# Kernel optimization log

Measured on AMD Instinct MI355X. Metric: run time of the kernel, lower is better.

Reference implementation:

```python
import jax, jax.numpy as jnp
import numpy as np

N, CH, H, W = 2, 64, 96, 96
NH, CHUNK, RED = 4, 144, 4
CM = CH // RED  # match channels = 16
RES_SCALE = 1.0
NORM_EPS = 5e-5


def conv2d(x, w, b):
    # 3x3 'same' conv, NCHW / OIHW
    y = jax.lax.conv_general_dilated(x, w, (1, 1), 'SAME',
                                     dimension_numbers=('NCHW', 'OIHW', 'NCHW'))
    return y + b[None, :, None, None]


def setup_inputs() -> dict:
    key = jax.random.key(0)
    ks = jax.random.split(key, 8)
    L = H * W
    hb = min(L // CHUNK + (L // CHUNK) % 2, 128)  # = 64
    x = jax.random.normal(ks[0], (N, CH, H, W), jnp.float32)
    # per-round semi-orthogonal rotations: rows of (CM, hb) orthonormal
    g = jax.random.normal(ks[1], (NH, hb, CM), jnp.float32)
    q = jnp.stack([jnp.linalg.qr(g[h])[0] for h in range(NH)])  # (NH, hb, CM)
    rot = jnp.transpose(q, (2, 0, 1))  # (CM, NH, hb)
    def s(k, shape, fan):
        return jax.random.normal(k, shape, jnp.float32) / np.sqrt(fan).astype(np.float32)
    wm = s(ks[2], (CM, CH, 3, 3), CH * 9)
    wa = s(ks[3], (CH, CH, 3, 3), CH * 9)
    wf = s(ks[4], (CH, CH, 3, 3), CH * 9)
    fc1_w = s(ks[5], (CHUNK, CH), CH)
    fc2_w = s(ks[6], (CHUNK, CHUNK), CHUNK)
    return {'x': x, 'rot': rot,
            'wm': wm, 'bm': jnp.zeros((CM,), jnp.float32),
            'wa': wa, 'ba': jnp.zeros((CH,), jnp.float32),
            'wf': wf, 'bf': jnp.zeros((CH,), jnp.float32),
            'fc1_w': fc1_w, 'fc1_b': jnp.zeros((CHUNK,), jnp.float32),
            'fc2_w': fc2_w, 'fc2_b': jnp.zeros((CHUNK,), jnp.float32)}


def reference(x, rot, wm, bm, wa, ba, wf, bf, fc1_w, fc1_b, fc2_w, fc2_b):
    n, _, h, w = x.shape
    L = h * w
    hb = rot.shape[-1]
    # embeddings: (N, L, C)
    xe = jax.nn.relu(conv2d(x, wm, bm)).reshape(n, CM, L).transpose(0, 2, 1)
    ye = jax.nn.relu(conv2d(x, wa, ba)).reshape(n, CH, L).transpose(0, 2, 1)
    fe = jax.nn.relu(conv2d(x, wf, bf)).reshape(n, CH, L).transpose(0, 2, 1)
    # LSH: argmax over rotated directions, offset per round (detached in original)
    rv = jnp.einsum('ntf,fhi->nhti', xe, rot)  # (N, NH, L, hb)
    codes = jnp.argmax(rv, -1) + (jnp.arange(NH) * hb)[None, :, None]
    codes = codes.reshape(n, NH * L)
    idx = jnp.argsort(codes, axis=-1)
    undo = jnp.argsort(idx, axis=-1)
    mod = idx % L
    gather = lambda t: jnp.take_along_axis(t, mod[..., None], axis=1)
    nch = L // CHUNK  # L chosen divisible by CHUNK -> padding = 0
    xs = gather(xe).reshape(n, NH, nch, CHUNK, CM)
    ys = gather(ye).reshape(n, NH, nch, CHUNK, CH)
    fs = gather(fe).reshape(n, NH, nch, CHUNK, CH)
    nrm = jnp.linalg.norm(xs, axis=-1, keepdims=True)
    xmatch = xs / jnp.maximum(nrm, NORM_EPS)
    adj = lambda t: jnp.concatenate([t, jnp.roll(t, 1, axis=2), jnp.roll(t, -1, axis=2)], axis=3)
    xmatch = adj(xmatch)   # (n, NH, nch, 3*CHUNK, CM)
    ya = adj(ys)           # (n, NH, nch, 3*CHUNK, CH)
    fa = adj(fs)           # (n, NH, nch, 3*CHUNK, CH)
    hid = jax.nn.relu(fa @ fc1_w.T + fc1_b)
    fc_raw = jnp.swapaxes(hid @ fc2_w.T + fc2_b, -1, -2)  # (n, NH, nch, CHUNK, 3*CHUNK)
    raw = jnp.einsum('nhkie,nhkje->nhkij', xs, xmatch) + fc_raw
    bsc = jax.scipy.special.logsumexp(raw, axis=-1, keepdims=True)
    score = jnp.exp(raw - bsc)
    ret = jnp.einsum('nhkij,nhkje->nhkie', score, ya)  # (n, NH, nch, CHUNK, CH)
    ret = ret.reshape(n, NH * L, CH)
    bsc = bsc.reshape(n, NH * L)
    ret = jnp.take_along_axis(ret, undo[..., None], axis=1)
    bsc = jnp.take_along_axis(bsc, undo, axis=1)
    ret = ret.reshape(n, NH, L, CH)
    probs = jax.nn.softmax(bsc.reshape(n, NH, L, 1), axis=1)
    out = jnp.sum(ret * probs, axis=1)  # (n, L, CH)
    out = out.transpose(0, 2, 1).reshape(n, CH, h, w)
    return out * RES_SCALE + x
```

## Files before the change

kernel.cpp:

```cpp
#include <hip/hip_runtime.h>
#include <hip/hip_bf16.h>

#define LL 9216
#define TOT 36864
#define CHK 144
#define NSEG 144
#define EPS_N 5e-5f

typedef __bf16 bf16x8 __attribute__((ext_vector_type(8)));
typedef float f32x4 __attribute__((ext_vector_type(4)));

__device__ __forceinline__ float dot4(float4 a, float4 b) {
    return a.x*b.x + a.y*b.y + a.z*b.z + a.w*b.w;
}
__device__ __forceinline__ unsigned short f2bf(float f) {
    __hip_bfloat16 h = __float2bfloat16(f);
    return *reinterpret_cast<unsigned short*>(&h);
}
__device__ __forceinline__ float bf2f(unsigned short u) {
    return __uint_as_float(((unsigned int)u) << 16);
}

__global__ __launch_bounds__(256) void k_wprep(
    const float* __restrict__ fc1w, const float* __restrict__ fc2w,
    const float* __restrict__ wa, const float* __restrict__ wf,
    unsigned short* __restrict__ w1bf, unsigned short* __restrict__ w2bf,
    unsigned short* __restrict__ wpack)
{
    int i = blockIdx.x * 256 + threadIdx.x;
    if (i < 144 * 64) w1bf[i] = f2bf(fc1w[i]);
    if (i < 144 * 160) {
        int r = i / 160, c = i - r * 160;
        w2bf[i] = (c < 144) ? f2bf(fc2w[r * 144 + c]) : 0;
    }
    if (i < 128 * 576) {
        int o = i / 576, kk = i - o * 576;
        int dydx = kk >> 6, c = kk & 63;
        const float* src = (o < 64) ? wa : wf;
        wpack[i] = f2bf(src[(o & 63) * 576 + c * 9 + dydx]);
    }
}

__global__ __launch_bounds__(256) void k_conv2(
    const float* __restrict__ x, const float* __restrict__ wm,
    const float* __restrict__ bm, const float* __restrict__ rot,
    unsigned short* __restrict__ xeb, unsigned short* __restrict__ xnb,
    unsigned char* __restrict__ codes,
    const unsigned short* __restrict__ wpack,
    const float* __restrict__ ba, const float* __restrict__ bfb,
    const unsigned short* __restrict__ w1bf, const float* __restrict__ fc1_b,
    const unsigned short* __restrict__ w2bf, const float* __restrict__ fc2_b,
    unsigned short* __restrict__ yeb, unsigned short* __restrict__ re2b)
{
    __shared__ __align__(16) char smem[47104];
    int tid = threadIdx.x;
    int b7 = blockIdx.x % 7, bq = blockIdx.x / 7;

    if (b7 < 3) {
        float* xl   = (float*)smem;
        float* rotT = (float*)(smem + 25600);
        float* xsp  = (float*)(smem + 41984);
        int b = bq * 3 + b7;
        int n = b / 144, tile = b % 144;
        int ty0 = (tile / 12) * 8, tx0 = (tile % 12) * 8;
        for (int li = tid; li < 6400; li += 256) {
            int c = li / 100, s = li % 100;
            int yy = s / 10, xx = s % 10;
            int gy = ty0 + yy - 1, gx = tx0 + xx - 1;
            float v = 0.f;
            if ((unsigned)gy < 96u && (unsigned)gx < 96u)
                v = x[((n * 64 + c) * 96 + gy) * 96 + gx];
            xl[li] = v;
        }
        for (int e = tid; e < 4096; e += 256) {
            int f = e >> 8, r = e & 255;
            rotT[r * 16 + f] = rot[f * 256 + r];
        }
        __syncthreads();
        int p = tid & 63, og = tid >> 6;
        int row = p >> 3, col = p & 7;
        int ogs = __builtin_amdgcn_readfirstlane(og);
        const float* wb = wm + (size_t)ogs * 4 * 576;
        float acc0 = 0.f, acc1 = 0.f, acc2 = 0.f, acc3 = 0.f;
        for (int c = 0; c < 64; ++c) {
            float xp[9];
            int base = c * 100 + row * 10 + col;
            #pragma unroll
            for (int dy = 0; dy < 3; ++dy)
                #pragma unroll
                for (int dx = 0; dx < 3; ++dx)
                    xp[dy * 3 + dx] = xl[base + dy * 10 + dx];
            const float* w0 = wb + c * 9;
            #pragma unroll
            for (int u = 0; u < 9; ++u) {
                acc0 += w0[u]        * xp[u];
                acc1 += w0[576 + u]  * xp[u];
                acc2 += w0[1152 + u] * xp[u];
                acc3 += w0[1728 + u] * xp[u];
            }
        }
        int o = ogs * 4;
        float v0 = acc0 + bm[o + 0]; v0 = v0 > 0.f ? v0 : 0.f;
        float v1 = acc1 + bm[o + 1]; v1 = v1 > 0.f ? v1 : 0.f;
        float v2 = acc2 + bm[o + 2]; v2 = v2 > 0.f ? v2 : 0.f;
        float v3 = acc3 + bm[o + 3]; v3 = v3 > 0.f ? v3 : 0.f;
        size_t t = (size_t)n * LL + (ty0 + row) * 96 + tx0 + col;
        unsigned short pk[4] = {f2bf(v0), f2bf(v1), f2bf(v2), f2bf(v3)};
        *(uint2*)(xeb + t * 16 + o) = *(uint2*)pk;
        *(float4*)(xsp + p * 20 + o) = make_float4(v0, v1, v2, v3);
        __syncthreads();
        int pos = tid & 63, h = tid >> 6;
        int prow = pos >> 3, pcol = pos & 7;
        size_t tc = (size_t)n * LL + (ty0 + prow) * 96 + tx0 + pcol;
        float4 q0 = *(float4*)(xsp + pos * 20 + 0);
        float4 q1 = *(float4*)(xsp + pos * 20 + 4);
        float4 q2 = *(float4*)(xsp + pos * 20 + 8);
        float4 q3 = *(float4*)(xsp + pos * 20 + 12);
        if (h == 0) {
            float nn = dot4(q0,q0) + dot4(q1,q1) + dot4(q2,q2) + dot4(q3,q3);
            float s = fmaxf(sqrtf(nn), EPS_N);
            float inv = 1.f / s;
            unsigned short pn[16];
            pn[0]=f2bf(q0.x*inv);  pn[1]=f2bf(q0.y*inv);  pn[2]=f2bf(q0.z*inv);  pn[3]=f2bf(q0.w*inv);
            pn[4]=f2bf(q1.x*inv);  pn[5]=f2bf(q1.y*inv);  pn[6]=f2bf(q1.z*inv);  pn[7]=f2bf(q1.w*inv);
            pn[8]=f2bf(q2.x*inv);  pn[9]=f2bf(q2.y*inv);  pn[10]=f2bf(q2.z*inv); pn[11]=f2bf(q2.w*inv);
            pn[12]=f2bf(q3.x*inv); pn[13]=f2bf(q3.y*inv); pn[14]=f2bf(q3.z*inv); pn[15]=f2bf(q3.w*inv);
            *(uint4*)(xnb + tc * 16)     = ((uint4*)pn)[0];
            *(uint4*)(xnb + tc * 16 + 8) = ((uint4*)pn)[1];
        }
        float best = -1e30f; int bi = 0;
        const float* rp = rotT + h * 1024;
        for (int i = 0; i < 64; ++i) {
            const float4* r4 = (const float4*)(rp + i * 16);
            float v = dot4(q0, r4[0]) + dot4(q1, r4[1]) + dot4(q2, r4[2]) + dot4(q3, r4[3]);
            if (v > best) { best = v; bi = i; }
        }
        codes[(size_t)n * TOT + h * LL + (tc - (size_t)n * LL)] = (unsigned char)(h * 64 + bi);
        return;
    }

    unsigned short* xt  = (unsigned short*)smem;
    unsigned short* fet = (unsigned short*)(smem + 21600);
    unsigned short* hb  = (unsigned short*)(smem + 28512);
    int b = bq * 4 + (b7 - 3);
    int n = b / 192, rem = b % 192;
    int y = rem >> 1, strip = rem & 1;
    int x0 = strip * 48;
    for (int e = tid; e < 9600; e += 256) {
        int r = e / 3200, r2 = e - r * 3200;
        int c = r2 / 50, j = r2 - c * 50;
        int gy = y - 1 + r, gx = x0 - 1 + j;
        float v = 0.f;
        if ((unsigned)gy < 96u && (unsigned)gx < 96u)
            v = x[((n * 64 + c) * 96 + gy) * 96 + gx];
        xt[(r * 50 + j) * 72 + c] = f2bf(v);
    }
    for (int e = tid; e < 384; e += 256) {
        int r = e >> 3, pq = e & 7;
        *(unsigned int*)(hb + r * 168 + 144 + pq * 2) = 0;
    }
    __syncthreads();
    int wave = tid >> 6, lane = tid & 63;
    int n16 = lane & 15, quad = lane >> 4;
    f32x4 acc[2][3];
    #pragma unroll
    for (int mi = 0; mi < 2; ++mi)
        #pragma unroll
        for (int nt = 0; nt < 3; ++nt) acc[mi][nt] = (f32x4){0.f, 0.f, 0.f, 0.f};
    #pragma unroll
    for (int s = 0; s < 18; ++s) {
        int dydx = s >> 1, half = s & 1;
        int dy = dydx / 3, dxm = dydx - dy * 3;
        bf16x8 B[3];
        #pragma unroll
        for (int nt = 0; nt < 3; ++nt) {
            int j = nt * 16 + n16 + dxm;
            B[nt] = *(bf16x8*)(xt + (dy * 50 + j) * 72 + half * 32 + quad * 8);
        }
        #pragma unroll
        for (int mi = 0; mi < 2; ++mi) {
            int o = (wave * 2 + mi) * 16 + n16;
            bf16x8 A = *(const bf16x8*)(wpack + o * 576 + dydx * 64 + half * 32 + quad * 8);
            #pragma unroll
            for (int nt = 0; nt < 3; ++nt)
                acc[mi][nt] = __builtin_amdgcn_mfma_f32_16x16x32_bf16(A, B[nt], acc[mi][nt], 0, 0, 0);
        }
    }
    #pragma unroll
    for (int mi = 0; mi < 2; ++mi) {
        int mt = wave * 2 + mi;
        int obase = mt * 16 + quad * 4;
        float4 b4 = (mt < 4) ? *(const float4*)(ba + obase)
                             : *(const float4*)(bfb + obase - 64);
        #pragma unroll
        for (int nt = 0; nt < 3; ++nt) {
            int j = nt * 16 + n16;
            unsigned short pk[4];
            float v0 = acc[mi][nt][0] + b4.x; pk[0] = f2bf(v0 > 0.f ? v0 : 0.f);
            float v1 = acc[mi][nt][1] + b4.y; pk[1] = f2bf(v1 > 0.f ? v1 : 0.f);
            float v2 = acc[mi][nt][2] + b4.z; pk[2] = f2bf(v2 > 0.f ? v2 : 0.f);
            float v3 = acc[mi][nt][3] + b4.w; pk[3] = f2bf(v3 > 0.f ? v3 : 0.f);
            if (mt < 4) {
                size_t t = (size_t)n * LL + y * 96 + x0 + j;
                *(uint2*)(yeb + t * 64 + obase) = *(uint2*)pk;
            } else {
                *(uint2*)(fet + j * 72 + (obase - 64)) = *(uint2*)pk;
            }
        }
    }
    __syncthreads();
    size_t R0 = (size_t)n * LL + y * 96 + x0;
    for (int nt = wave; nt < 9; nt += 4) {
        int bn = nt * 16 + n16;
        bf16x8 b0 = *(const bf16x8*)(w1bf + bn * 64 + quad * 8);
        bf16x8 b1 = *(const bf16x8*)(w1bf + bn * 64 + 32 + quad * 8);
        float bb = fc1_b[bn];
        #pragma unroll
        for (int m = 0; m < 3; ++m) {
            int arow = m * 16 + n16;
            bf16x8 a0 = *(bf16x8*)(fet + arow * 72 + quad * 8);
            bf16x8 a1 = *(bf16x8*)(fet + arow * 72 + 32 + quad * 8);
            f32x4 c2 = {0.f, 0.f, 0.f, 0.f};
            c2 = __builtin_amdgcn_mfma_f32_16x16x32_bf16(a0, b0, c2, 0, 0, 0);
            c2 = __builtin_amdgcn_mfma_f32_16x16x32_bf16(a1, b1, c2, 0, 0, 0);
            #pragma unroll
            for (int r = 0; r < 4; ++r) {
                float v = c2[r] + bb;
                hb[(m * 16 + quad * 4 + r) * 168 + bn] = f2bf(v > 0.f ? v : 0.f);
            }
        }
    }
    __syncthreads();
    for (int nt = wave; nt < 9; nt += 4) {
        int bn = nt * 16 + n16;
        bf16x8 wv2[5];
        #pragma unroll
        for (int kk = 0; kk < 5; ++kk)
            wv2[kk] = *(const bf16x8*)(w2bf + bn * 160 + kk * 32 + quad * 8);
        float bb = fc2_b[bn];
        #pragma unroll
        for (int m = 0; m < 3; ++m) {
            int arow = m * 16 + n16;
            f32x4 c2 = {0.f, 0.f, 0.f, 0.f};
            #pragma unroll
            for (int kk = 0; kk < 5; ++kk) {
                bf16x8 a = *(bf16x8*)(hb + arow * 168 + kk * 32 + quad * 8);
                c2 = __builtin_amdgcn_mfma_f32_16x16x32_bf16(a, wv2[kk], c2, 0, 0, 0);
            }
            #pragma unroll
            for (int r = 0; r < 4; ++r)
                re2b[(R0 + m * 16 + quad * 4 + r) * 144 + bn] = f2bf(c2[r] + bb);
        }
    }
}

__global__ __launch_bounds__(256) void k_hist(
    const unsigned char* __restrict__ codes, int* __restrict__ hist)
{
    __shared__ int lh[256];
    int b2 = blockIdx.x;
    int n = b2 / NSEG, seg = b2 % NSEG;
    int tid = threadIdx.x;
    lh[tid] = 0;
    __syncthreads();
    int code = codes[(size_t)n * TOT + seg * 256 + tid];
    atomicAdd(&lh[code], 1);
    __syncthreads();
    hist[((size_t)n * 256 + tid) * NSEG + seg] = lh[tid];
}

__global__ __launch_bounds__(256, 1) void k_scan(int* __restrict__ hist)
{
    __shared__ int sc[256];
    int n = blockIdx.x, bin = threadIdx.x;
    int* hp = hist + ((size_t)n * 256 + bin) * NSEG;
    int4 buf[36];
    int4* hp4 = (int4*)hp;
    #pragma unroll
    for (int q = 0; q < 36; ++q) buf[q] = hp4[q];
    int running = 0;
    #pragma unroll
    for (int q = 0; q < 36; ++q) {
        int t0 = buf[q].x; buf[q].x = running; running += t0;
        int t1 = buf[q].y; buf[q].y = running; running += t1;
        int t2 = buf[q].z; buf[q].z = running; running += t2;
        int t3 = buf[q].w; buf[q].w = running; running += t3;
    }
    sc[bin] = running;
    __syncthreads();
    for (int off = 1; off < 256; off <<= 1) {
        int v = sc[bin];
        int u = (bin >= off) ? sc[bin - off] : 0;
        __syncthreads();
        sc[bin] = v + u;
        __syncthreads();
    }
    int bs = sc[bin] - running;
    #pragma unroll
    for (int q = 0; q < 36; ++q) {
        buf[q].x += bs; buf[q].y += bs; buf[q].z += bs; buf[q].w += bs;
        hp4[q] = buf[q];
    }
}

__global__ __launch_bounds__(256) void k_place(
    const unsigned char* __restrict__ codes, const int* __restrict__ hist,
    int* __restrict__ idx)
{
    __shared__ unsigned char cl[256];
    __shared__ int wh[4][256];
    int b = blockIdx.x, n = b / NSEG, seg = b % NSEG;
    int tid = threadIdx.x, wv = tid >> 6;
    for (int e = tid; e < 1024; e += 256) ((int*)wh)[e] = 0;
    int my = codes[(size_t)n * TOT + seg * 256 + tid];
    cl[tid] = (unsigned char)my;
    __syncthreads();
    atomicAdd(&wh[wv][my], 1);
    __syncthreads();
    int rank = 0;
    for (int j = wv << 6; j < tid; ++j) rank += (cl[j] == my);
    #pragma unroll
    for (int w = 0; w < 3; ++w)
        if (w < wv) rank += wh[w][my];
    int pos = hist[((size_t)n * 256 + my) * NSEG + seg] + rank;
    idx[(size_t)n * TOT + pos] = seg * 256 + tid;
}

__global__ __launch_bounds__(256) void k_gather(
    const int* __restrict__ idx, const unsigned short* __restrict__ xeb,
    const unsigned short* __restrict__ xnb, const unsigned short* __restrict__ yeb,
    const unsigned short* __restrict__ re2b,
    unsigned short* __restrict__ qs, unsigned short* __restrict__ ks,
    unsigned short* __restrict__ vsT, unsigned short* __restrict__ fst,
    int* __restrict__ undo)
{
    __shared__ int tl[144];
    int b0 = blockIdx.x;
    int half = b0 >> 9, bb = b0 & 511;
    int b = ((bb & 7) << 6) | (bb >> 3);
    int nh = b >> 6, chunk = b & 63;
    int n = nh >> 2, h = nh & 3;
    size_t gb = (size_t)nh * LL + chunk * 144;
    size_t nL = (size_t)n * LL;
    int tid = threadIdx.x;
    if (tid < 144) {
        int t = idx[(size_t)n * TOT + h * LL + chunk * 144 + tid] - h * LL;
        tl[tid] = t;
        if (half) undo[(size_t)nh * LL + t] = chunk * 144 + tid;
    }
    __syncthreads();
    if (!half) {
        for (int e = tid; e < 288; e += 256) {
            int s = e >> 1, hf = e & 1;
            size_t src = (nL + tl[s]) * 16 + hf * 8;
            *(uint4*)(qs + (gb + s) * 16 + hf * 8) = *(const uint4*)(xeb + src);
            *(uint4*)(ks + (gb + s) * 16 + hf * 8) = *(const uint4*)(xnb + src);
        }
        size_t vb = (size_t)(nh * 64 + chunk) * 64;
        for (int e = tid; e < 576; e += 256) {
            int p = e % 72, su = e / 72;
            uint4 a  = *(const uint4*)(yeb + (nL + tl[2 * p])     * 64 + su * 8);
            uint4 bq = *(const uint4*)(yeb + (nL + tl[2 * p + 1]) * 64 + su * 8);
            const unsigned short* pa = (const unsigned short*)&a;
            const unsigned short* pb = (const unsigned short*)&bq;
            #pragma unroll
            for (int ci = 0; ci < 8; ++ci) {
                int c = su * 8 + ci;
                *(unsigned int*)(vsT + (vb + c) * 144 + 2 * p) =
                    (unsigned int)pa[ci] | ((unsigned int)pb[ci] << 16);
            }
        }
    } else {
        for (int e = tid; e < 1296; e += 256) {
            int mt = e / 144, s = e - mt * 144;
            const unsigned short* src = re2b + (nL + tl[s]) * 144 + mt * 16;
            unsigned short* dst = fst + ((size_t)(nh * 9 + mt) * LL + chunk * 144 + s) * 16;
            *(uint4*)(dst)     = *(const uint4*)(src);
            *(uint4*)(dst + 8) = *(const uint4*)(src + 8);
        }
    }
}

__global__ __launch_bounds__(256, 2) void k_attn(
    const unsigned short* __restrict__ qs, const unsigned short* __restrict__ ks,
    const unsigned short* __restrict__ vsT, const unsigned short* __restrict__ fst,
    unsigned short* __restrict__ rets, float* __restrict__ bscs)
{
    __shared__ __align__(16) unsigned short Pw[4][16 * 56];

    int B = blockIdx.x;
    int wb = (B & 7) * 144 + (B >> 3);
    int tid = threadIdx.x;
    int lane = tid & 63, wv = tid >> 6;
    int n16 = lane & 15, quad = lane >> 4;
    int job = wb * 4 + wv;
    int bucket = job / 9, mt = job - bucket * 9;
    int n = bucket >> 8, rem = bucket & 255;
    int h = rem >> 6, k = rem & 63;
    int nh = n * 4 + h;

    size_t hL = (size_t)nh * LL;
    int ch0 = k, ch1 = (k + 63) & 63, ch2 = (k + 1) & 63;
    unsigned short* Pp = &Pw[wv][0];
    const unsigned short* fsl = fst + (size_t)(nh * 9 + mt) * LL * 16;

    bf16x8 afragQ = {};
    if (quad < 2)
        afragQ = *(const bf16x8*)(qs + (hL + ch0 * 144 + mt * 16 + n16) * 16 + quad * 8);

    f32x4 acc[4];
    float rm[4], rl[4];
    #pragma unroll
    for (int ct = 0; ct < 4; ++ct) acc[ct] = (f32x4){0.f, 0.f, 0.f, 0.f};
    #pragma unroll
    for (int r = 0; r < 4; ++r) { rm[r] = -1e30f; rl[r] = 0.f; }

#define SLOT(T) ((((T) < 3) ? ch0 : ((T) < 6) ? ch1 : ch2) * 144 + ((T) % 3) * 48)

#define LOAD_KF(T, KS, FV) do {                                                      \
    int sl_ = SLOT(T);                                                               \
    if (quad < 2) {                                                                  \
        KS[0] = *(const bf16x8*)(ks + (hL + sl_ + n16) * 16 + quad * 8);             \
        KS[1] = *(const bf16x8*)(ks + (hL + sl_ + 16 + n16) * 16 + quad * 8);        \
        KS[2] = *(const bf16x8*)(ks + (hL + sl_ + 32 + n16) * 16 + quad * 8);        \
    }                                                                                \
    FV[0] = *(const ushort4*)(fsl + (size_t)(sl_ + n16) * 16 + quad * 4);            \
    FV[1] = *(const ushort4*)(fsl + (size_t)(sl_ + 16 + n16) * 16 + quad * 4);       \
    FV[2] = *(const ushort4*)(fsl + (size_t)(sl_ + 32 + n16) * 16 + quad * 4);       \
} while (0)

#define ATTN_ITER(T, KS, FV, NKS, NFV) do {                                          \
    int chx_ = ((T) < 3) ? ch0 : ((T) < 6) ? ch1 : ch2;                              \
    const unsigned short* vch_ = vsT + (size_t)(nh * 64 + chx_) * 9216;              \
    int vo_ = ((T) % 3) * 48;                                                        \
    bf16x8 Bv0_[4];                                                                  \
    _Pragma("unroll")                                                                \
    for (int ct_ = 0; ct_ < 4; ++ct_)                                                \
        Bv0_[ct_] = *(const bf16x8*)(vch_ + (size_t)(ct_ * 16 + n16) * 144 + vo_ + quad * 8); \
    if ((T) < 8) LOAD_KF((T) + 1, NKS, NFV);                                         \
    f32x4 c0_ = {bf2f(FV[0].x), bf2f(FV[0].y), bf2f(FV[0].z), bf2f(FV[0].w)};        \
    f32x4 c1_ = {bf2f(FV[1].x), bf2f(FV[1].y), bf2f(FV[1].z), bf2f(FV[1].w)};        \
    f32x4 c2_ = {bf2f(FV[2].x), bf2f(FV[2].y), bf2f(FV[2].z), bf2f(FV[2].w)};        \
    c0_ = __builtin_amdgcn_mfma_f32_16x16x32_bf16(afragQ, KS[0], c0_, 0, 0, 0);      \
    c1_ = __builtin_amdgcn_mfma_f32_16x16x32_bf16(afragQ, KS[1], c1_, 0, 0, 0);      \
    c2_ = __builtin_amdgcn_mfma_f32_16x16x32_bf16(afragQ, KS[2], c2_, 0, 0, 0);      \
    _Pragma("unroll")                                                                \
    for (int r_ = 0; r_ < 4; ++r_) {                                                 \
        float v0_ = c0_[r_], v1_ = c1_[r_], v2_ = c2_[r_];                           \
        float mm_ = fmaxf(fmaxf(v0_, v1_), v2_);                                     \
        mm_ = fmaxf(mm_, __shfl_xor(mm_, 1, 16));                                    \
        mm_ = fmaxf(mm_, __shfl_xor(mm_, 2, 16));                                    \
        mm_ = fmaxf(mm_, __shfl_xor(mm_, 4, 16));                                    \
        mm_ = fmaxf(mm_, __shfl_xor(mm_, 8, 16));                                    \
        float mn_ = fmaxf(rm[r_], mm_);                                              \
        float a_ = __expf(rm[r_] - mn_);                                             \
        float s0_ = __expf(v0_ - mn_), s1_ = __expf(v1_ - mn_), s2_ = __expf(v2_ - mn_); \
        float ss_ = s0_ + s1_ + s2_;                                                 \
        ss_ += __shfl_xor(ss_, 1, 16);                                               \
        ss_ += __shfl_xor(ss_, 2, 16);                                               \
        ss_ += __shfl_xor(ss_, 4, 16);                                               \
        ss_ += __shfl_xor(ss_, 8, 16);                                               \
        rl[r_] = rl[r_] * a_ + ss_;                                                  \
        rm[r_] = mn_;                                                                \
        acc[0][r_] *= a_; acc[1][r_] *= a_; acc[2][r_] *= a_; acc[3][r_] *= a_;      \
        int rw_ = quad * 4 + r_;                                                     \
        Pp[rw_ * 56 +      n16] = f2bf(s0_);                                         \
        Pp[rw_ * 56 + 16 + n16] = f2bf(s1_);                                         \
        Pp[rw_ * 56 + 32 + n16] = f2bf(s2_);                                         \
    }                                                                                \
                \
    bf16x8 Ap0_ = *(const bf16x8*)(Pp + n16 * 56 + quad * 8);                        \
    int ko1_ = (quad < 2) ? 32 + quad * 8 : 0;          \
    bf16x8 Bv1_[4];                                                                  \
    _Pragma("unroll")                                                                \
    for (int ct_ = 0; ct_ < 4; ++ct_)                                                \
        Bv1_[ct_] = *(const bf16x8*)(vch_ + (size_t)(ct_ * 16 + n16) * 144 + vo_ + ko1_); \
    _Pragma("unroll")                                                                \
    for (int ct_ = 0; ct_ < 4; ++ct_)                                                \
        acc[ct_] = __builtin_amdgcn_mfma_f32_16x16x32_bf16(Ap0_, Bv0_[ct_], acc[ct_], 0, 0, 0); \
    bf16x8 Ap1_ = {};                                                                \
    if (quad < 2)                                                                    \
        Ap1_ = *(const bf16x8*)(Pp + n16 * 56 + 32 + quad * 8);                      \
    _Pragma("unroll")                                                                \
    for (int ct_ = 0; ct_ < 4; ++ct_)                                                \
        acc[ct_] = __builtin_amdgcn_mfma_f32_16x16x32_bf16(Ap1_, Bv1_[ct_], acc[ct_], 0, 0, 0); \
} while (0)

    bf16x8 ksA[3] = {}, ksB[3] = {};
    ushort4 fvA[3], fvB[3];
    LOAD_KF(0, ksA, fvA);
    ATTN_ITER(0, ksA, fvA, ksB, fvB);
    ATTN_ITER(1, ksB, fvB, ksA, fvA);
    ATTN_ITER(2, ksA, fvA, ksB, fvB);
    ATTN_ITER(3, ksB, fvB, ksA, fvA);
    ATTN_ITER(4, ksA, fvA, ksB, fvB);
    ATTN_ITER(5, ksB, fvB, ksA, fvA);
    ATTN_ITER(6, ksA, fvA, ksB, fvB);
    ATTN_ITER(7, ksB, fvB, ksA, fvA);
    ATTN_ITER(8, ksA, fvA, ksB, fvB);

#undef ATTN_ITER
#undef LOAD_KF
#undef SLOT

    size_t sp0 = hL + ch0 * 144;
    if (n16 == 0) {
        #pragma unroll
        for (int r = 0; r < 4; ++r)
            bscs[sp0 + mt * 16 + quad * 4 + r] = rm[r] + __logf(rl[r]);
    }
    #pragma unroll
    for (int r = 0; r < 4; ++r) {
        float inv = 1.f / rl[r];
        #pragma unroll
        for (int ct = 0; ct < 4; ++ct)
            rets[(sp0 + mt * 16 + quad * 4 + r) * 64 + ct * 16 + n16] =
                f2bf(acc[ct][r] * inv);
    }
}

__global__ __launch_bounds__(256) void k_final(
    const unsigned short* __restrict__ rets, const float* __restrict__ bscs,
    const int* __restrict__ undo, const float* __restrict__ x,
    float* __restrict__ out)
{
    __shared__ float pr[4][16];
    __shared__ int us[4][16];
    __shared__ float accl[64 * 17];
    int b = blockIdx.x, n = b / 576;
    int t0 = (b % 576) * 16;
    int tid = threadIdx.x;
    if (tid < 64) {
        int h = tid >> 4, tt = tid & 15;
        us[h][tt] = undo[((size_t)n * 4 + h) * LL + t0 + tt];
    }
    __syncthreads();
    if (tid < 16) {
        float b0 = bscs[((size_t)n * 4 + 0) * LL + us[0][tid]];
        float b1 = bscs[((size_t)n * 4 + 1) * LL + us[1][tid]];
        float b2 = bscs[((size_t)n * 4 + 2) * LL + us[2][tid]];
        float b3 = bscs[((size_t)n * 4 + 3) * LL + us[3][tid]];
        float mx = fmaxf(fmaxf(b0, b1), fmaxf(b2, b3));
        float e0 = __expf(b0-mx), e1 = __expf(b1-mx), e2 = __expf(b2-mx), e3 = __expf(b3-mx);
        float inv = 1.f / (e0 + e1 + e2 + e3);
        pr[0][tid] = e0*inv; pr[1][tid] = e1*inv; pr[2][tid] = e2*inv; pr[3][tid] = e3*inv;
    }
    __syncthreads();
    int cc = tid & 63, tq = tid >> 6;
    #pragma unroll
    for (int q = 0; q < 4; ++q) {
        int tt = tq * 4 + q;
        float v = 0.f;
        #pragma unroll
        for (int h2 = 0; h2 < 4; ++h2)
            v += bf2f(rets[(((size_t)n*4 + h2)*LL + us[h2][tt])*64 + cc]) * pr[h2][tt];
        accl[cc*17 + tt] = v;
    }
    __syncthreads();
    int tt = tid & 15, c4 = tid >> 4;
    #pragma unroll
    for (int q = 0; q < 4; ++q) {
        int ch = c4 + 16*q;
        size_t o = ((size_t)n*64 + ch)*LL + t0 + tt;
        out[o] = accl[ch*17 + tt] + x[o];
    }
}

extern "C" void kernel_launch(void* const* d_in, const int* in_sizes, int n_in,
                              void* d_out, int out_size, void* d_ws, size_t ws_size,
                              hipStream_t stream)
{
    const float* x    = (const float*)d_in[0];
    const float* rot  = (const float*)d_in[1];
    const float* wm   = (const float*)d_in[2];
    const float* bm   = (const float*)d_in[3];
    const float* wa   = (const float*)d_in[4];
    const float* ba   = (const float*)d_in[5];
    const float* wf   = (const float*)d_in[6];
    const float* bf   = (const float*)d_in[7];
    const float* fc1w = (const float*)d_in[8];
    const float* fc1b = (const float*)d_in[9];
    const float* fc2w = (const float*)d_in[10];
    const float* fc2b = (const float*)d_in[11];
    float* out = (float*)d_out;

    char* ws = (char*)d_ws;
    unsigned short* xeb  = (unsigned short*)(ws + 0);
    unsigned short* yeb  = (unsigned short*)(ws + 589824);
    unsigned short* xnb  = (unsigned short*)(ws + 2949120);
    unsigned short* re2b = (unsigned short*)(ws + 3538944);
    unsigned short* w1bf = (unsigned short*)(ws + 8847360);
    unsigned short* w2bf = (unsigned short*)(ws + 8865792);
    unsigned short* wpak = (unsigned short*)(ws + 8911872);
    unsigned char* codes = (unsigned char*)(ws + 9059328);
    int* hist            = (int*)(ws + 9133056);
    int* idxb            = (int*)(ws + 9427968);
    unsigned short* rets = (unsigned short*)(ws + 0);
    float* bscs          = (float*)(ws + 9437184);
    unsigned short* qs   = (unsigned short*)(ws + 9732096);
    unsigned short* ks   = (unsigned short*)(ws + 12091392);
    unsigned short* vsT  = (unsigned short*)(ws + 14450688);
    unsigned short* fst  = (unsigned short*)(ws + 23887872);
    int* undo            = (int*)(ws + 45121536);

    k_wprep    <<<288,  256, 0, stream>>>(fc1w, fc2w, wa, wf, w1bf, w2bf, wpak);
    k_conv2    <<<672,  256, 0, stream>>>(x, wm, bm, rot, xeb, xnb, codes,
                                          wpak, ba, bf, w1bf, fc1b, w2bf, fc2b,
                                          yeb, re2b);
    k_hist     <<<288,  256, 0, stream>>>(codes, hist);
    k_scan     <<<2,    256, 0, stream>>>(hist);
    k_place    <<<288,  256, 0, stream>>>(codes, hist, idxb);
    k_gather   <<<1024, 256, 0, stream>>>(idxb, xeb, xnb, yeb, re2b,
                                          qs, ks, vsT, fst, undo);
    k_attn     <<<1152, 256, 0, stream>>>(qs, ks, vsT, fst, rets, bscs);
    k_final    <<<1152, 256, 0, stream>>>(rets, bscs, undo, x, out);
}
```

Before: 190.1 us.

## Widen conv kernel to 512 threads, split LSH argmax and pack two row-strips per block

The fused conv kernel moves from 256 to 512-thread blocks. The match-conv path now gives each wave 2 output channels instead of 4, and splits each round's 64-way LSH argmax across two waves, merging the halves through shared memory. The MFMA conv path runs two independent 256-thread halves per block, each handling its own row strip with a separate shared-memory slice. The hb buffer now aliases xt, so zeroing its padding moves after the conv barrier. The aim is shorter per-thread serial work and fewer blocks, at the cost of more shared memory per block, an extra barrier and possibly lower occupancy.

```diff
diff --git a/kernel.cpp b/kernel.cpp
--- a/kernel.cpp
+++ b/kernel.cpp
@@ -41,7 +41,7 @@
     }
 }
 
-__global__ __launch_bounds__(256) void k_conv2(
+__global__ __launch_bounds__(512) void k_conv2(
     const float* __restrict__ x, const float* __restrict__ wm,
     const float* __restrict__ bm, const float* __restrict__ rot,
     unsigned short* __restrict__ xeb, unsigned short* __restrict__ xnb,
@@ -52,18 +52,20 @@
     const unsigned short* __restrict__ w2bf, const float* __restrict__ fc2_b,
     unsigned short* __restrict__ yeb, unsigned short* __restrict__ re2b)
 {
-    __shared__ __align__(16) char smem[47104];
+    __shared__ __align__(16) char smem[57024];
     int tid = threadIdx.x;
-    int b7 = blockIdx.x % 7, bq = blockIdx.x / 7;
-
-    if (b7 < 3) {
-        float* xl   = (float*)smem;
-        float* rotT = (float*)(smem + 25600);
-        float* xsp  = (float*)(smem + 41984);
-        int b = bq * 3 + b7;
+    int b5 = blockIdx.x % 5, bq = blockIdx.x / 5;
+
+    if (b5 < 3) {
+        float* xl     = (float*)smem;
+        float* rotT   = (float*)(smem + 25600);
+        float* xsp    = (float*)(smem + 41984);
+        float* bestsh = (float*)(smem + 47104);
+        int*   bish   = (int*)  (smem + 49152);
+        int b = bq * 3 + b5;
         int n = b / 144, tile = b % 144;
         int ty0 = (tile / 12) * 8, tx0 = (tile % 12) * 8;
-        for (int li = tid; li < 6400; li += 256) {
+        for (int li = tid; li < 6400; li += 512) {
             int c = li / 100, s = li % 100;
             int yy = s / 10, xx = s % 10;
             int gy = ty0 + yy - 1, gx = tx0 + xx - 1;
@@ -72,16 +74,16 @@
                 v = x[((n * 64 + c) * 96 + gy) * 96 + gx];
             xl[li] = v;
         }
-        for (int e = tid; e < 4096; e += 256) {
+        for (int e = tid; e < 4096; e += 512) {
             int f = e >> 8, r = e & 255;
             rotT[r * 16 + f] = rot[f * 256 + r];
         }
         __syncthreads();
-        int p = tid & 63, og = tid >> 6;
+        int p = tid & 63, wv = tid >> 6;
         int row = p >> 3, col = p & 7;
-        int ogs = __builtin_amdgcn_readfirstlane(og);
-        const float* wb = wm + (size_t)ogs * 4 * 576;
-        float acc0 = 0.f, acc1 = 0.f, acc2 = 0.f, acc3 = 0.f;
+        int wvs = __builtin_amdgcn_readfirstlane(wv);
+        const float* wb = wm + (size_t)wvs * 2 * 576;
+        float acc0 = 0.f, acc1 = 0.f;
         for (int c = 0; c < 64; ++c) {
             float xp[9];
             int base = c * 100 + row * 10 + col;
@@ -93,30 +95,27 @@
             const float* w0 = wb + c * 9;
             #pragma unroll
             for (int u = 0; u < 9; ++u) {
-                acc0 += w0[u]        * xp[u];
-                acc1 += w0[576 + u]  * xp[u];
-                acc2 += w0[1152 + u] * xp[u];
-                acc3 += w0[1728 + u] * xp[u];
+                acc0 += w0[u]       * xp[u];
+                acc1 += w0[576 + u] * xp[u];
             }
         }
-        int o = ogs * 4;
+        int o = wvs * 2;
         float v0 = acc0 + bm[o + 0]; v0 = v0 > 0.f ? v0 : 0.f;
         float v1 = acc1 + bm[o + 1]; v1 = v1 > 0.f ? v1 : 0.f;
-        float v2 = acc2 + bm[o + 2]; v2 = v2 > 0.f ? v2 : 0.f;
-        float v3 = acc3 + bm[o + 3]; v3 = v3 > 0.f ? v3 : 0.f;
         size_t t = (size_t)n * LL + (ty0 + row) * 96 + tx0 + col;
-        unsigned short pk[4] = {f2bf(v0), f2bf(v1), f2bf(v2), f2bf(v3)};
-        *(uint2*)(xeb + t * 16 + o) = *(uint2*)pk;
-        *(float4*)(xsp + p * 20 + o) = make_float4(v0, v1, v2, v3);
+        unsigned short pk[2] = {f2bf(v0), f2bf(v1)};
+        *(unsigned int*)(xeb + t * 16 + o) = *(unsigned int*)pk;
+        *(float2*)(xsp + p * 20 + o) = make_float2(v0, v1);
         __syncthreads();
-        int pos = tid & 63, h = tid >> 6;
+        int pos = tid & 63, g = tid >> 6;
+        int h = g & 3, dh = g >> 2;
         int prow = pos >> 3, pcol = pos & 7;
         size_t tc = (size_t)n * LL + (ty0 + prow) * 96 + tx0 + pcol;
         float4 q0 = *(float4*)(xsp + pos * 20 + 0);
         float4 q1 = *(float4*)(xsp + pos * 20 + 4);
         float4 q2 = *(float4*)(xsp + pos * 20 + 8);
         float4 q3 = *(float4*)(xsp + pos * 20 + 12);
-        if (h == 0) {
+        if (g == 0) {
             float nn = dot4(q0,q0) + dot4(q1,q1) + dot4(q2,q2) + dot4(q3,q3);
             float s = fmaxf(sqrtf(nn), EPS_N);
             float inv = 1.f / s;
@@ -129,24 +128,35 @@
             *(uint4*)(xnb + tc * 16 + 8) = ((uint4*)pn)[1];
         }
         float best = -1e30f; int bi = 0;
-        const float* rp = rotT + h * 1024;
-        for (int i = 0; i < 64; ++i) {
+        const float* rp = rotT + h * 1024 + dh * 512;
+        for (int i = 0; i < 32; ++i) {
             const float4* r4 = (const float4*)(rp + i * 16);
             float v = dot4(q0, r4[0]) + dot4(q1, r4[1]) + dot4(q2, r4[2]) + dot4(q3, r4[3]);
             if (v > best) { best = v; bi = i; }
         }
-        codes[(size_t)n * TOT + h * LL + (tc - (size_t)n * LL)] = (unsigned char)(h * 64 + bi);
+        bestsh[pos * 8 + g] = best;
+        bish[pos * 8 + g] = bi;
+        __syncthreads();
+        if (dh == 0) {
+            float b1 = bestsh[pos * 8 + g + 4];
+            int   i1 = bish[pos * 8 + g + 4];
+            int fbi = (b1 > best) ? (i1 + 32) : bi;
+            codes[(size_t)n * TOT + h * LL + (tc - (size_t)n * LL)] =
+                (unsigned char)(h * 64 + fbi);
+        }
         return;
     }
 
-    unsigned short* xt  = (unsigned short*)smem;
-    unsigned short* fet = (unsigned short*)(smem + 21600);
-    unsigned short* hb  = (unsigned short*)(smem + 28512);
-    int b = bq * 4 + (b7 - 3);
+    int hid = tid >> 8, tid2 = tid & 255;
+    char* sl = smem + hid * 28512;
+    unsigned short* xt  = (unsigned short*)sl;
+    unsigned short* hb  = (unsigned short*)sl;
+    unsigned short* fet = (unsigned short*)(sl + 21600);
+    int b = (bq * 2 + (b5 - 3)) * 2 + hid;
     int n = b / 192, rem = b % 192;
     int y = rem >> 1, strip = rem & 1;
     int x0 = strip * 48;
-    for (int e = tid; e < 9600; e += 256) {
+    for (int e = tid2; e < 9600; e += 256) {
         int r = e / 3200, r2 = e - r * 3200;
         int c = r2 / 50, j = r2 - c * 50;
         int gy = y - 1 + r, gx = x0 - 1 + j;
@@ -155,12 +165,8 @@
             v = x[((n * 64 + c) * 96 + gy) * 96 + gx];
         xt[(r * 50 + j) * 72 + c] = f2bf(v);
     }
-    for (int e = tid; e < 384; e += 256) {
-        int r = e >> 3, pq = e & 7;
-        *(unsigned int*)(hb + r * 168 + 144 + pq * 2) = 0;
-    }
-    __syncthreads();
-    int wave = tid >> 6, lane = tid & 63;
+    __syncthreads();
+    int wave = tid2 >> 6, lane = tid2 & 63;
     int n16 = lane & 15, quad = lane >> 4;
     f32x4 acc[2][3];
     #pragma unroll
@@ -209,6 +215,10 @@
         }
     }
     __syncthreads();
+    for (int e = tid2; e < 384; e += 256) {
+        int r = e >> 3, pq = e & 7;
+        *(unsigned int*)(hb + r * 168 + 144 + pq * 2) = 0;
+    }
     size_t R0 = (size_t)n * LL + y * 96 + x0;
     for (int nt = wave; nt < 9; nt += 4) {
         int bn = nt * 16 + n16;
@@ -604,7 +614,7 @@
     int* undo            = (int*)(ws + 45121536);
 
     k_wprep    <<<288,  256, 0, stream>>>(fc1w, fc2w, wa, wf, w1bf, w2bf, wpak);
-    k_conv2    <<<672,  256, 0, stream>>>(x, wm, bm, rot, xeb, xnb, codes,
+    k_conv2    <<<480,  512, 0, stream>>>(x, wm, bm, rot, xeb, xnb, codes,
                                           wpak, ba, bf, w1bf, fc1b, w2bf, fc2b,
                                           yeb, re2b);
     k_hist     <<<288,  256, 0, stream>>>(codes, hist);
```

Measured after the change: 194.8 us. 1.02x slower.
